# Optimization experiments

Hardware: AMD Instinct MI355X
Metric: run time of the kernel (lower is better)

## Reference

```python
import jax, jax.numpy as jnp
import numpy as np

H_DIM = 1024
HEAD_DIM = 128
N_HEADS = 8
HD = HEAD_DIM * N_HEADS  # 1024


def setup_inputs() -> dict:
    key = jax.random.key(0)
    ks = jax.random.split(key, 32)
    B, S = 16, 1024
    inp = {
        "f_in": jax.random.normal(ks[0], (B, S, H_DIM), jnp.float32),
        "i_in": jax.random.normal(ks[1], (B, S, H_DIM), jnp.float32),
        "z_in": jax.random.normal(ks[2], (B, S, H_DIM), jnp.float32),
        "o_in": jax.random.normal(ks[3], (B, S, H_DIM), jnp.float32),
        "c0": jax.random.normal(ks[4], (B, N_HEADS, HEAD_DIM), jnp.float32),
        "h0": jax.random.normal(ks[5], (B, N_HEADS, HEAD_DIM), jnp.float32),
    }
    # Parameters (torch Linear stored here as [in, out]; init std=0.02, zero bias)
    names_x = ["Fx", "Ix", "Zx", "Ox"]
    names_h = ["Fh", "Ih", "Zh", "Oh"]
    for j, n in enumerate(names_x):
        inp[f"W_{n}"] = 0.02 * jax.random.normal(ks[6 + j], (H_DIM, HD), jnp.float32)
        inp[f"b_{n}"] = jnp.zeros((HD,), jnp.float32)
    for j, n in enumerate(names_h):
        inp[f"W_{n}"] = 0.02 * jax.random.normal(ks[10 + j], (HD, HD), jnp.float32)
        inp[f"b_{n}"] = jnp.zeros((HD,), jnp.float32)
    inp["W_post"] = 0.02 * jax.random.normal(ks[14], (HD, H_DIM), jnp.float32)
    inp["b_post"] = jnp.zeros((H_DIM,), jnp.float32)
    return inp


def reference(f_in, i_in, z_in, o_in, c0, h0,
              W_Fx, b_Fx, W_Ix, b_Ix, W_Zx, b_Zx, W_Ox, b_Ox,
              W_Fh, b_Fh, W_Ih, b_Ih, W_Zh, b_Zh, W_Oh, b_Oh,
              W_post, b_post):
    B, S, _ = f_in.shape
    # Precompute input-to-gate projections for all timesteps: (B,S,HD)
    fx = f_in @ W_Fx + b_Fx
    ix = i_in @ W_Ix + b_Ix
    zx = z_in @ W_Zx + b_Zx
    ox = o_in @ W_Ox + b_Ox
    # Flatten head state: gating is elementwise, heads are contiguous in HD
    c = c0.reshape(B, HD)
    h = h0.reshape(B, HD)
    # Time-major for scan: (S,B,HD)
    xs = (fx.transpose(1, 0, 2), ix.transpose(1, 0, 2),
          zx.transpose(1, 0, 2), ox.transpose(1, 0, 2))

    def step(carry, x):
        c, h = carry
        fx_t, ix_t, zx_t, ox_t = x
        f = jax.nn.sigmoid(fx_t + h @ W_Fh + b_Fh)
        i = jax.nn.sigmoid(ix_t + h @ W_Ih + b_Ih)
        z = jnp.tanh(zx_t + h @ W_Zh + b_Zh)
        o = jax.nn.sigmoid(ox_t + h @ W_Oh + b_Oh)
        c = f * c + i * z
        h = o * jnp.tanh(c)
        return (c, h), h

    (c, h), ys = jax.lax.scan(step, (c, h), xs)
    y = ys.transpose(1, 0, 2)  # (B,S,HD)
    y = y @ W_post + b_post    # n_heads > 1 -> post-head projection
    state = (c.reshape(B, N_HEADS, HEAD_DIM), h.reshape(B, N_HEADS, HEAD_DIM))
    return (y, state)
```

## Files before the change

kernel.cpp:

```cpp
#include <hip/hip_runtime.h>
#include <stdint.h>
#include <stddef.h>

typedef __attribute__((ext_vector_type(8))) short short8;
typedef __attribute__((ext_vector_type(4))) short short4_t;
typedef __attribute__((ext_vector_type(8))) unsigned short ushort8_t;
typedef __attribute__((ext_vector_type(4))) unsigned short ushort4_t;
typedef __attribute__((ext_vector_type(4))) float f32x4;
typedef __attribute__((ext_vector_type(4))) unsigned uint4_t;

#define XG_BYTES  (134217728ull)
#define HS_BYTES  (33587200ull)
#define FLAGS_OFF (XG_BYTES + HS_BYTES)
#define WT_OFF    (FLAGS_OFF + 32768ull)

#define SENT 0x7FC07FC0u

__device__ __forceinline__ unsigned short f2b(float f){
  unsigned u = __builtin_bit_cast(unsigned, f);
  u += 0x7fffu + ((u >> 16) & 1u);
  return (unsigned short)(u >> 16);
}
__device__ __forceinline__ float b2f(unsigned short b){
  unsigned u = ((unsigned)b) << 16;
  return __builtin_bit_cast(float, u);
}
__device__ __forceinline__ float sigm(float x){ return 1.0f / (1.0f + __expf(-x)); }
__device__ __forceinline__ float tanh_(float x){ return 2.0f / (1.0f + __expf(-2.0f*x)) - 1.0f; }

__device__ __forceinline__ void ld_h8_mall(const unsigned short* p, short8* a){
  asm volatile(
    "global_load_dwordx4 %0, %8, off sc0 sc1\n\t"
    "global_load_dwordx4 %1, %8, off offset:64 sc0 sc1\n\t"
    "global_load_dwordx4 %2, %8, off offset:128 sc0 sc1\n\t"
    "global_load_dwordx4 %3, %8, off offset:192 sc0 sc1\n\t"
    "global_load_dwordx4 %4, %8, off offset:256 sc0 sc1\n\t"
    "global_load_dwordx4 %5, %8, off offset:320 sc0 sc1\n\t"
    "global_load_dwordx4 %6, %8, off offset:384 sc0 sc1\n\t"
    "global_load_dwordx4 %7, %8, off offset:448 sc0 sc1\n\t"
    "s_waitcnt vmcnt(0)"
    : "=&v"(a[0]), "=&v"(a[1]), "=&v"(a[2]), "=&v"(a[3]),
      "=&v"(a[4]), "=&v"(a[5]), "=&v"(a[6]), "=&v"(a[7])
    : "v"(p) : "memory");
}
__device__ __forceinline__ void st_u32_mall(unsigned* p, unsigned v){
  asm volatile("global_store_dword %0, %1, off sc0 sc1"
               :: "v"(p), "v"(v) : "memory");
}

__global__ __launch_bounds__(256) void k_prep(
    const float* __restrict__ w0, const float* __restrict__ w1,
    const float* __restrict__ w2, const float* __restrict__ w3,
    const float* __restrict__ w4, const float* __restrict__ w5,
    const float* __restrict__ w6, const float* __restrict__ w7,
    const float* __restrict__ w8, unsigned short* __restrict__ wt)
{
  const int z = blockIdx.z;
  const float* W = (z==0)?w0:(z==1)?w1:(z==2)?w2:(z==3)?w3:(z==4)?w4:
                   (z==5)?w5:(z==6)?w6:(z==7)?w7:w8;
  unsigned short* out = wt + (size_t)z*1024*1024;
  __shared__ float tile[64][65];
  const int k0 = blockIdx.x*64, n0 = blockIdx.y*64;
  const int tid = threadIdx.x;
  {
    const int kk = tid >> 2, nn0 = (tid & 3) * 16;
    const float* src = W + (size_t)(k0+kk)*1024 + n0 + nn0;
    #pragma unroll
    for (int j=0;j<16;j+=4){
      f32x4 v = *(const f32x4*)(src + j);
      tile[kk][nn0+j+0]=v[0]; tile[kk][nn0+j+1]=v[1];
      tile[kk][nn0+j+2]=v[2]; tile[kk][nn0+j+3]=v[3];
    }
  }
  __syncthreads();
  {
    const int nn = tid >> 2, kk0 = (tid & 3) * 16;
    ushort8_t a, b;
    #pragma unroll
    for (int j=0;j<8;++j){ a[j]=f2b(tile[kk0+j][nn]); b[j]=f2b(tile[kk0+8+j][nn]); }
    unsigned short* dst = out + (size_t)(n0+nn)*1024 + k0 + kk0;
    *(ushort8_t*)dst = a;
    *(ushort8_t*)(dst+8) = b;
  }
}

__global__ void k_init(const float* __restrict__ h0, unsigned short* __restrict__ hs){
  const int i = blockIdx.x*256 + threadIdx.x;
  hs[i] = f2b(h0[i]);
}

__global__ void k_fill(unsigned* __restrict__ hsw){
  const size_t i = (size_t)blockIdx.x*256 + threadIdx.x;
  uint4_t v = (uint4_t){SENT, SENT, SENT, SENT};
  *(uint4_t*)(hsw + 8192 + i*4) = v;
}

__global__ __launch_bounds__(256,2) void k_xproj(
    const float* __restrict__ xF, const float* __restrict__ xI,
    const float* __restrict__ xZ, const float* __restrict__ xO,
    const float* __restrict__ bF, const float* __restrict__ bI,
    const float* __restrict__ bZ, const float* __restrict__ bO,
    const unsigned short* __restrict__ Wt,
    unsigned short* __restrict__ xg)
{
  const int g  = blockIdx.z;
  const int tm = blockIdx.x, tn = blockIdx.y;
  const float* X  = (g==0)?xF:(g==1)?xI:(g==2)?xZ:xO;
  const float* Bp = (g==0)?bF:(g==1)?bI:(g==2)?bZ:bO;
  const unsigned short* Wg = Wt + (size_t)g*1024*1024;

  __shared__ unsigned short Asm[128*32];
  __shared__ unsigned short Bsm[128*32];

  const int tid  = threadIdx.x;
  const int lane = tid & 63, wv = tid >> 6;
  const int l15  = lane & 15, lg = lane >> 4;
  const int wy   = wv >> 1,  wx = wv & 1;

  const int rr = tid >> 1, kq = tid & 1;
  const int ar = tm*128 + rr;
  const int ab = ar & 15, as_ = ar >> 4;
  const float* aptr = X + ((size_t)ab*1024 + as_)*1024 + kq*16;
  const unsigned short* bp_ = Wg + (size_t)(tn*128 + rr)*1024 + kq*16;
  const int s0 = kq*2;
  unsigned short* aw0 = &Asm[rr*32 + (((s0  ) ^ (rr&3))<<3)];
  unsigned short* aw1 = &Asm[rr*32 + (((s0+1) ^ (rr&3))<<3)];
  unsigned short* bw0 = &Bsm[rr*32 + (((s0  ) ^ (rr&3))<<3)];
  unsigned short* bw1 = &Bsm[rr*32 + (((s0+1) ^ (rr&3))<<3)];

  f32x4 acc[4][4];
  #pragma unroll
  for (int m=0;m<4;++m)
    #pragma unroll
    for (int q=0;q<4;++q) acc[m][q] = (f32x4){0.f,0.f,0.f,0.f};

  for (int k0=0; k0<1024; k0+=32){
    const float* ap = aptr + k0;
    f32x4 v0 = *(const f32x4*)(ap + 0);
    f32x4 v1 = *(const f32x4*)(ap + 4);
    f32x4 v2 = *(const f32x4*)(ap + 8);
    f32x4 v3 = *(const f32x4*)(ap + 12);
    ushort8_t pa, pb;
    #pragma unroll
    for (int j=0;j<4;++j){ pa[j]=f2b(v0[j]); pa[4+j]=f2b(v1[j]); pb[j]=f2b(v2[j]); pb[4+j]=f2b(v3[j]); }
    *(ushort8_t*)aw0 = pa;
    *(ushort8_t*)aw1 = pb;
    ushort8_t q0 = *(const ushort8_t*)(bp_ + k0);
    ushort8_t q1 = *(const ushort8_t*)(bp_ + k0 + 8);
    *(ushort8_t*)bw0 = q0;
    *(ushort8_t*)bw1 = q1;
    __syncthreads();

    short8 af[4], bf_[4];
    #pragma unroll
    for (int m=0;m<4;++m){
      int row = wy*64 + m*16 + l15;
      af[m] = *(const short8*)&Asm[row*32 + ((lg ^ (row&3))<<3)];
    }
    #pragma unroll
    for (int q=0;q<4;++q){
      int row = wx*64 + q*16 + l15;
      bf_[q] = *(const short8*)&Bsm[row*32 + ((lg ^ (row&3))<<3)];
    }
    #pragma unroll
    for (int m=0;m<4;++m)
      #pragma unroll
      for (int q=0;q<4;++q)
        acc[m][q] = __builtin_amdgcn_mfma_f32_16x16x32_bf16(af[m], bf_[q], acc[m][q], 0,0,0);
    __syncthreads();
  }

  #pragma unroll
  for (int m=0;m<4;++m){
    const int t = tm*8 + wy*4 + m;
    #pragma unroll
    for (int q=0;q<4;++q){
      const int n = tn*128 + wx*64 + q*16 + l15;
      const float bias = Bp[n];
      f32x4 v = acc[m][q];
      ushort4_t pk;
      #pragma unroll
      for (int r=0;r<4;++r) pk[r] = f2b(v[r] + bias);
      *(ushort4_t*)(xg + (size_t)((t*4+g)*1024 + n)*16 + lg*4) = pk;
    }
  }
}

__global__ __launch_bounds__(256,1) void k_recur(
    const unsigned short* __restrict__ WtR,
    const float* __restrict__ bfh, const float* __restrict__ bih,
    const float* __restrict__ bzh, const float* __restrict__ boh,
    const float* __restrict__ c0,
    const unsigned short* __restrict__ xg,
    unsigned short* __restrict__ hs,
    float* __restrict__ oc, float* __restrict__ oh)
{
  const int wg   = blockIdx.x;
  const int tid  = threadIdx.x;
  const int wv   = tid >> 6, lane = tid & 63;
  const int l15  = lane & 15, lg = lane >> 4;
  const int n    = wg*16 + l15;

  short8 wf[4][8];
  #pragma unroll
  for (int g=0; g<4; ++g){
    const unsigned short* wp = WtR + (size_t)g*1048576 + (size_t)n*1024 + wv*256 + lg*8;
    #pragma unroll
    for (int c=0; c<8; ++c)
      wf[g][c] = *(const short8*)(wp + c*32);
  }

  float cst[4]; float bias[4];
  bias[0]=bfh[n]; bias[1]=bih[n]; bias[2]=bzh[n]; bias[3]=boh[n];
  #pragma unroll
  for (int r=0;r<4;++r) cst[r] = c0[(size_t)(lg*4+r)*1024 + n];

  __shared__ f32x4 part[2][4][4][64];

  unsigned* hsw = (unsigned*)hs;

  for (int t=0; t<1024; ++t){
    short4_t xq[4];
    #pragma unroll
    for (int g=0; g<4; ++g)
      xq[g] = *(const short4_t*)(xg + (size_t)((t*4+g)*1024 + n)*16 + lg*4);

    const unsigned short* hp = hs + (size_t)t*16384 + (size_t)l15*1024 + wv*256 + lg*8;
    short8 a[8];
    ld_h8_mall(hp, a);
    for(;;){
      bool bad = false;
      #pragma unroll
      for (int c=0;c<8;++c){
        uint4_t q = __builtin_bit_cast(uint4_t, a[c]);
        bad |= (q[0]==SENT)|(q[1]==SENT)|(q[2]==SENT)|(q[3]==SENT);
      }
      if (!__any(bad)) break;
      __builtin_amdgcn_s_sleep(1);
      ld_h8_mall(hp, a);
    }

    f32x4 acc[4];
    #pragma unroll
    for (int g=0;g<4;++g) acc[g] = (f32x4){0.f,0.f,0.f,0.f};
    #pragma unroll
    for (int c=0;c<8;++c){
      acc[0] = __builtin_amdgcn_mfma_f32_16x16x32_bf16(a[c], wf[0][c], acc[0], 0,0,0);
      acc[1] = __builtin_amdgcn_mfma_f32_16x16x32_bf16(a[c], wf[1][c], acc[1], 0,0,0);
      acc[2] = __builtin_amdgcn_mfma_f32_16x16x32_bf16(a[c], wf[2][c], acc[2], 0,0,0);
      acc[3] = __builtin_amdgcn_mfma_f32_16x16x32_bf16(a[c], wf[3][c], acc[3], 0,0,0);
    }
    const int pb = t & 1;
    #pragma unroll
    for (int g=0;g<4;++g) part[pb][wv][g][lane] = acc[g];
    __syncthreads();

    f32x4 r_[4];
    #pragma unroll
    for (int g=0;g<4;++g){
      f32x4 s0 = part[pb][0][g][lane];
      f32x4 s1 = part[pb][1][g][lane];
      f32x4 s2 = part[pb][2][g][lane];
      f32x4 s3 = part[pb][3][g][lane];
      r_[g] = (s0 + s1) + (s2 + s3);
    }

    float hv[4];
    {
      const int r = wv;
      float pf = r_[0][r] + b2f((unsigned short)xq[0][r]) + bias[0];
      float pi = r_[1][r] + b2f((unsigned short)xq[1][r]) + bias[1];
      float pz = r_[2][r] + b2f((unsigned short)xq[2][r]) + bias[2];
      float po = r_[3][r] + b2f((unsigned short)xq[3][r]) + bias[3];
      float fg = sigm(pf), ig = sigm(pi), zg = tanh_(pz), og = sigm(po);
      float cn = fg*cst[r] + ig*zg;
      cst[r] = cn;
      hv[r] = og * tanh_(cn);
      unsigned m  = (unsigned)f2b(hv[r]);
      unsigned nb = (unsigned)__shfl_xor(m, 1);
      if ((l15 & 1) == 0){
        unsigned word = m | (nb << 16);
        unsigned* pw = hsw + (size_t)(t+1)*8192 + (size_t)(lg*4+wv)*512 + (n >> 1);
        st_u32_mall(pw, word);
      }
    }
    #pragma unroll
    for (int r=0;r<4;++r){
      if (r == wv) continue;
      float pf = r_[0][r] + b2f((unsigned short)xq[0][r]) + bias[0];
      float pi = r_[1][r] + b2f((unsigned short)xq[1][r]) + bias[1];
      float pz = r_[2][r] + b2f((unsigned short)xq[2][r]) + bias[2];
      float po = r_[3][r] + b2f((unsigned short)xq[3][r]) + bias[3];
      float fg = sigm(pf), ig = sigm(pi), zg = tanh_(pz), og = sigm(po);
      float cn = fg*cst[r] + ig*zg;
      cst[r] = cn;
      hv[r] = og * tanh_(cn);
    }
    if (t == 1023 && wv == 0){
      #pragma unroll
      for (int r=0;r<4;++r){
        oc[(size_t)(lg*4+r)*1024 + n] = cst[r];
        oh[(size_t)(lg*4+r)*1024 + n] = hv[r];
      }
    }
  }
}

__global__ __launch_bounds__(256,2) void k_post(
    const unsigned short* __restrict__ hs,
    const unsigned short* __restrict__ Wt,
    const float* __restrict__ bpost,
    float* __restrict__ y)
{
  const int tm = blockIdx.x, tn = blockIdx.y;
  __shared__ unsigned short Asm[128*32];
  __shared__ unsigned short Bsm[128*32];

  const int tid  = threadIdx.x;
  const int lane = tid & 63, wv = tid >> 6;
  const int l15  = lane & 15, lg = lane >> 4;
  const int wy   = wv >> 1,  wx = wv & 1;

  const int rr = tid >> 1, kq = tid & 1;
  const unsigned short* aptr = hs + 16384 + (size_t)(tm*128 + rr)*1024 + kq*16;
  const unsigned short* bp_  = Wt + (size_t)4*1024*1024 + (size_t)(tn*128 + rr)*1024 + kq*16;
  const int s0 = kq*2;
  unsigned short* aw0 = &Asm[rr*32 + (((s0  ) ^ (rr&3))<<3)];
  unsigned short* aw1 = &Asm[rr*32 + (((s0+1) ^ (rr&3))<<3)];
  unsigned short* bw0 = &Bsm[rr*32 + (((s0  ) ^ (rr&3))<<3)];
  unsigned short* bw1 = &Bsm[rr*32 + (((s0+1) ^ (rr&3))<<3)];

  f32x4 acc[4][4];
  #pragma unroll
  for (int m=0;m<4;++m)
    #pragma unroll
    for (int q=0;q<4;++q) acc[m][q] = (f32x4){0.f,0.f,0.f,0.f};

  for (int k0=0; k0<1024; k0+=32){
    ushort8_t a0 = *(const ushort8_t*)(aptr + k0);
    ushort8_t a1 = *(const ushort8_t*)(aptr + k0 + 8);
    *(ushort8_t*)aw0 = a0;
    *(ushort8_t*)aw1 = a1;
    ushort8_t q0 = *(const ushort8_t*)(bp_ + k0);
    ushort8_t q1 = *(const ushort8_t*)(bp_ + k0 + 8);
    *(ushort8_t*)bw0 = q0;
    *(ushort8_t*)bw1 = q1;
    __syncthreads();

    short8 af[4], bf_[4];
    #pragma unroll
    for (int m=0;m<4;++m){
      int row = wy*64 + m*16 + l15;
      af[m] = *(const short8*)&Asm[row*32 + ((lg ^ (row&3))<<3)];
    }
    #pragma unroll
    for (int q=0;q<4;++q){
      int row = wx*64 + q*16 + l15;
      bf_[q] = *(const short8*)&Bsm[row*32 + ((lg ^ (row&3))<<3)];
    }
    #pragma unroll
    for (int m=0;m<4;++m)
      #pragma unroll
      for (int q=0;q<4;++q)
        acc[m][q] = __builtin_amdgcn_mfma_f32_16x16x32_bf16(af[m], bf_[q], acc[m][q], 0,0,0);
    __syncthreads();
  }

  #pragma unroll
  for (int m=0;m<4;++m){
    const int s = tm*8 + wy*4 + m;
    #pragma unroll
    for (int q=0;q<4;++q){
      const int n = tn*128 + wx*64 + q*16 + l15;
      const float bias = bpost[n];
      f32x4 v = acc[m][q];
      #pragma unroll
      for (int r=0;r<4;++r){
        const int b = lg*4 + r;
        y[((size_t)b << 20) + ((size_t)s << 10) + n] = v[r] + bias;
      }
    }
  }
}

extern "C" void kernel_launch(void* const* d_in, const int* in_sizes, int n_in,
                              void* d_out, int out_size, void* d_ws, size_t ws_size,
                              hipStream_t stream)
{
  const float* f_in = (const float*)d_in[0];
  const float* i_in = (const float*)d_in[1];
  const float* z_in = (const float*)d_in[2];
  const float* o_in = (const float*)d_in[3];
  const float* c0   = (const float*)d_in[4];
  const float* h0   = (const float*)d_in[5];
  const float* W_Fx = (const float*)d_in[6];  const float* b_Fx = (const float*)d_in[7];
  const float* W_Ix = (const float*)d_in[8];  const float* b_Ix = (const float*)d_in[9];
  const float* W_Zx = (const float*)d_in[10]; const float* b_Zx = (const float*)d_in[11];
  const float* W_Ox = (const float*)d_in[12]; const float* b_Ox = (const float*)d_in[13];
  const float* W_Fh = (const float*)d_in[14]; const float* b_Fh = (const float*)d_in[15];
  const float* W_Ih = (const float*)d_in[16]; const float* b_Ih = (const float*)d_in[17];
  const float* W_Zh = (const float*)d_in[18]; const float* b_Zh = (const float*)d_in[19];
  const float* W_Oh = (const float*)d_in[20]; const float* b_Oh = (const float*)d_in[21];
  const float* W_post = (const float*)d_in[22]; const float* b_post = (const float*)d_in[23];

  char* ws = (char*)d_ws;
  unsigned short* xg    = (unsigned short*)(ws);
  unsigned short* hs    = (unsigned short*)(ws + XG_BYTES);
  unsigned short* wt    = (unsigned short*)(ws + WT_OFF);

  float* y  = (float*)d_out;
  float* oc = y + 16777216;
  float* oh = oc + 16384;

  k_prep<<<dim3(16,16,9), 256, 0, stream>>>(W_Fx, W_Ix, W_Zx, W_Ox, W_post,
                                            W_Fh, W_Ih, W_Zh, W_Oh, wt);
  k_init<<<64, 256, 0, stream>>>(h0, hs);
  k_fill<<<8192, 256, 0, stream>>>((unsigned*)hs);
  k_xproj<<<dim3(128,8,4), 256, 0, stream>>>(f_in, i_in, z_in, o_in,
                                             b_Fx, b_Ix, b_Zx, b_Ox, wt, xg);
  k_recur<<<64, 256, 0, stream>>>(wt + (size_t)5*1024*1024,
                                  b_Fh, b_Ih, b_Zh, b_Oh,
                                  c0, xg, hs, oc, oh);
  k_post<<<dim3(128,8), 256, 0, stream>>>(hs, wt, b_post, y);
}
```

Baseline: 3.610 ms.

## Halve recurrent workgroups, add per-wave progress flags, prefetch next-step gate inputs

The recurrent kernel now runs on 32 workgroups instead of 64, and each workgroup handles 32 hidden columns, so every wave keeps twice as many weight fragments in registers. This halves the number of producers that must sync each timestep. Each wave gets a specific gate row to finish instead of computing all rows redundantly. Waiters now poll a small progress-flag array rather than sleeping and re-reading the whole h vector. The next timestep's x-projection values are prefetched during the MFMA phase, and the LDS partial-sum layout is changed to scalar floats. In exchange, each workgroup does twice the MFMA work per step and register pressure rises.

```diff
diff --git a/kernel.cpp b/kernel.cpp
--- a/kernel.cpp
+++ b/kernel.cpp
@@ -28,6 +28,13 @@
 __device__ __forceinline__ float sigm(float x){ return 1.0f / (1.0f + __expf(-x)); }
 __device__ __forceinline__ float tanh_(float x){ return 2.0f / (1.0f + __expf(-2.0f*x)) - 1.0f; }
 
+__device__ __forceinline__ unsigned ld_u32_mall(const unsigned* p){
+  unsigned v;
+  asm volatile("global_load_dword %0, %1, off sc0 sc1\n\t"
+               "s_waitcnt vmcnt(0)"
+               : "=v"(v) : "v"(p) : "memory");
+  return v;
+}
 __device__ __forceinline__ void ld_h8_mall(const unsigned short* p, short8* a){
   asm volatile(
     "global_load_dwordx4 %0, %8, off sc0 sc1\n\t"
@@ -193,38 +200,49 @@
     const float* __restrict__ c0,
     const unsigned short* __restrict__ xg,
     unsigned short* __restrict__ hs,
+    unsigned* __restrict__ flags,
     float* __restrict__ oc, float* __restrict__ oh)
 {
   const int wg   = blockIdx.x;
   const int tid  = threadIdx.x;
   const int wv   = tid >> 6, lane = tid & 63;
   const int l15  = lane & 15, lg = lane >> 4;
-  const int n    = wg*16 + l15;
-
-  short8 wf[4][8];
+  const int n0   = wg*32;
+  const int nA   = n0 + l15;
+  const int nB   = n0 + 16 + l15;
+  const int row  = lg*4 + wv;
+  const int sh   = wv * 16;
+
+  short8 wf[4][2][8];
+  #pragma unroll
+  for (int g=0; g<4; ++g)
+    #pragma unroll
+    for (int e=0; e<2; ++e){
+      const unsigned short* wp = WtR + (size_t)g*1048576
+                               + (size_t)(n0 + e*16 + l15)*1024 + wv*256 + lg*8;
+      #pragma unroll
+      for (int c=0; c<8; ++c)
+        wf[g][e][c] = *(const short8*)(wp + c*32);
+    }
+
+  float cstA = c0[(size_t)row*1024 + nA];
+  float cstB = c0[(size_t)row*1024 + nB];
+  float biasA[4] = {bfh[nA], bih[nA], bzh[nA], boh[nA]};
+  float biasB[4] = {bfh[nB], bih[nB], bzh[nB], boh[nB]};
+
+  __shared__ float part[2][4][4][2][4][64];
+
+  unsigned* hsw = (unsigned*)hs;
+
+  short4_t xqA[4], xqB[4];
   #pragma unroll
   for (int g=0; g<4; ++g){
-    const unsigned short* wp = WtR + (size_t)g*1048576 + (size_t)n*1024 + wv*256 + lg*8;
-    #pragma unroll
-    for (int c=0; c<8; ++c)
-      wf[g][c] = *(const short8*)(wp + c*32);
-  }
-
-  float cst[4]; float bias[4];
-  bias[0]=bfh[n]; bias[1]=bih[n]; bias[2]=bzh[n]; bias[3]=boh[n];
-  #pragma unroll
-  for (int r=0;r<4;++r) cst[r] = c0[(size_t)(lg*4+r)*1024 + n];
-
-  __shared__ f32x4 part[2][4][4][64];
-
-  unsigned* hsw = (unsigned*)hs;
-
+    xqA[g] = *(const short4_t*)(xg + (size_t)(g*1024 + nA)*16 + lg*4);
+    xqB[g] = *(const short4_t*)(xg + (size_t)(g*1024 + nB)*16 + lg*4);
+  }
+
+  float hvA = 0.f, hvB = 0.f;
   for (int t=0; t<1024; ++t){
-    short4_t xq[4];
-    #pragma unroll
-    for (int g=0; g<4; ++g)
-      xq[g] = *(const short4_t*)(xg + (size_t)((t*4+g)*1024 + n)*16 + lg*4);
-
     const unsigned short* hp = hs + (size_t)t*16384 + (size_t)l15*1024 + wv*256 + lg*8;
     short8 a[8];
     ld_h8_mall(hp, a);
@@ -236,74 +254,96 @@
         bad |= (q[0]==SENT)|(q[1]==SENT)|(q[2]==SENT)|(q[3]==SENT);
       }
       if (!__any(bad)) break;
-      __builtin_amdgcn_s_sleep(1);
+      unsigned fv;
+      do { fv = ld_u32_mall(flags + wv*32 + (lane & 31)); }
+      while (!__all((int)(fv >= (unsigned)t)));
       ld_h8_mall(hp, a);
     }
 
-    f32x4 acc[4];
-    #pragma unroll
-    for (int g=0;g<4;++g) acc[g] = (f32x4){0.f,0.f,0.f,0.f};
-    #pragma unroll
-    for (int c=0;c<8;++c){
-      acc[0] = __builtin_amdgcn_mfma_f32_16x16x32_bf16(a[c], wf[0][c], acc[0], 0,0,0);
-      acc[1] = __builtin_amdgcn_mfma_f32_16x16x32_bf16(a[c], wf[1][c], acc[1], 0,0,0);
-      acc[2] = __builtin_amdgcn_mfma_f32_16x16x32_bf16(a[c], wf[2][c], acc[2], 0,0,0);
-      acc[3] = __builtin_amdgcn_mfma_f32_16x16x32_bf16(a[c], wf[3][c], acc[3], 0,0,0);
-    }
+    short4_t xqA_n[4], xqB_n[4];
+    if (t < 1023){
+      const size_t tb = (size_t)(t+1)*4096;
+      #pragma unroll
+      for (int g=0; g<4; ++g){
+        xqA_n[g] = *(const short4_t*)(xg + (tb + (size_t)g*1024 + nA)*16 + lg*4);
+        xqB_n[g] = *(const short4_t*)(xg + (tb + (size_t)g*1024 + nB)*16 + lg*4);
+      }
+    }
+
+    f32x4 acc[4][2];
+    #pragma unroll
+    for (int g=0;g<4;++g){ acc[g][0]=(f32x4){0,0,0,0}; acc[g][1]=(f32x4){0,0,0,0}; }
+    #pragma unroll
+    for (int c=0;c<8;++c)
+      #pragma unroll
+      for (int g=0;g<4;++g){
+        acc[g][0] = __builtin_amdgcn_mfma_f32_16x16x32_bf16(a[c], wf[g][0][c], acc[g][0], 0,0,0);
+        acc[g][1] = __builtin_amdgcn_mfma_f32_16x16x32_bf16(a[c], wf[g][1][c], acc[g][1], 0,0,0);
+      }
+
     const int pb = t & 1;
     #pragma unroll
-    for (int g=0;g<4;++g) part[pb][wv][g][lane] = acc[g];
-    __syncthreads();
-
-    f32x4 r_[4];
+    for (int g=0;g<4;++g)
+      #pragma unroll
+      for (int e=0;e<2;++e)
+        #pragma unroll
+        for (int cm=0;cm<4;++cm)
+          part[pb][wv][g][e][cm][lane] = acc[g][e][cm];
+    asm volatile("s_waitcnt lgkmcnt(0)" ::: "memory");
+    __builtin_amdgcn_s_barrier();
+
+    float rgA[4], rgB[4];
     #pragma unroll
     for (int g=0;g<4;++g){
-      f32x4 s0 = part[pb][0][g][lane];
-      f32x4 s1 = part[pb][1][g][lane];
-      f32x4 s2 = part[pb][2][g][lane];
-      f32x4 s3 = part[pb][3][g][lane];
-      r_[g] = (s0 + s1) + (s2 + s3);
-    }
-
-    float hv[4];
+      rgA[g] = part[pb][0][g][0][wv][lane] + part[pb][1][g][0][wv][lane]
+             + part[pb][2][g][0][wv][lane] + part[pb][3][g][0][wv][lane];
+      rgB[g] = part[pb][0][g][1][wv][lane] + part[pb][1][g][1][wv][lane]
+             + part[pb][2][g][1][wv][lane] + part[pb][3][g][1][wv][lane];
+    }
+
     {
-      const int r = wv;
-      float pf = r_[0][r] + b2f((unsigned short)xq[0][r]) + bias[0];
-      float pi = r_[1][r] + b2f((unsigned short)xq[1][r]) + bias[1];
-      float pz = r_[2][r] + b2f((unsigned short)xq[2][r]) + bias[2];
-      float po = r_[3][r] + b2f((unsigned short)xq[3][r]) + bias[3];
+      float pf = rgA[0] + b2f((unsigned short)(__builtin_bit_cast(unsigned long long, xqA[0]) >> sh)) + biasA[0];
+      float pi = rgA[1] + b2f((unsigned short)(__builtin_bit_cast(unsigned long long, xqA[1]) >> sh)) + biasA[1];
+      float pz = rgA[2] + b2f((unsigned short)(__builtin_bit_cast(unsigned long long, xqA[2]) >> sh)) + biasA[2];
+      float po = rgA[3] + b2f((unsigned short)(__builtin_bit_cast(unsigned long long, xqA[3]) >> sh)) + biasA[3];
       float fg = sigm(pf), ig = sigm(pi), zg = tanh_(pz), og = sigm(po);
-      float cn = fg*cst[r] + ig*zg;
-      cst[r] = cn;
-      hv[r] = og * tanh_(cn);
-      unsigned m  = (unsigned)f2b(hv[r]);
-      unsigned nb = (unsigned)__shfl_xor(m, 1);
+      float cn = fg*cstA + ig*zg;
+      cstA = cn;
+      hvA = og * tanh_(cn);
+    }
+    {
+      float pf = rgB[0] + b2f((unsigned short)(__builtin_bit_cast(unsigned long long, xqB[0]) >> sh)) + biasB[0];
+      float pi = rgB[1] + b2f((unsigned short)(__builtin_bit_cast(unsigned long long, xqB[1]) >> sh)) + biasB[1];
+      float pz = rgB[2] + b2f((unsigned short)(__builtin_bit_cast(unsigned long long, xqB[2]) >> sh)) + biasB[2];
+      float po = rgB[3] + b2f((unsigned short)(__builtin_bit_cast(unsigned long long, xqB[3]) >> sh)) + biasB[3];
+      float fg = sigm(pf), ig = sigm(pi), zg = tanh_(pz), og = sigm(po);
+      float cn = fg*cstB + ig*zg;
+      cstB = cn;
+      hvB = og * tanh_(cn);
+    }
+
+    {
+      unsigned mA  = (unsigned)f2b(hvA);
+      unsigned nbA = (unsigned)__shfl_xor(mA, 1);
+      unsigned mB  = (unsigned)f2b(hvB);
+      unsigned nbB = (unsigned)__shfl_xor(mB, 1);
       if ((l15 & 1) == 0){
-        unsigned word = m | (nb << 16);
-        unsigned* pw = hsw + (size_t)(t+1)*8192 + (size_t)(lg*4+wv)*512 + (n >> 1);
-        st_u32_mall(pw, word);
+        unsigned* base = hsw + (size_t)(t+1)*8192 + (size_t)row*512;
+        st_u32_mall(base + (nA >> 1), mA | (nbA << 16));
+        st_u32_mall(base + (nB >> 1), mB | (nbB << 16));
       }
-    }
-    #pragma unroll
-    for (int r=0;r<4;++r){
-      if (r == wv) continue;
-      float pf = r_[0][r] + b2f((unsigned short)xq[0][r]) + bias[0];
-      float pi = r_[1][r] + b2f((unsigned short)xq[1][r]) + bias[1];
-      float pz = r_[2][r] + b2f((unsigned short)xq[2][r]) + bias[2];
-      float po = r_[3][r] + b2f((unsigned short)xq[3][r]) + bias[3];
-      float fg = sigm(pf), ig = sigm(pi), zg = tanh_(pz), og = sigm(po);
-      float cn = fg*cst[r] + ig*zg;
-      cst[r] = cn;
-      hv[r] = og * tanh_(cn);
-    }
-    if (t == 1023 && wv == 0){
-      #pragma unroll
-      for (int r=0;r<4;++r){
-        oc[(size_t)(lg*4+r)*1024 + n] = cst[r];
-        oh[(size_t)(lg*4+r)*1024 + n] = hv[r];
-      }
-    }
-  }
+      if (lane == 0)
+        st_u32_mall(flags + wg*4 + wv, (unsigned)(t+1));
+    }
+
+    #pragma unroll
+    for (int g=0; g<4; ++g){ xqA[g] = xqA_n[g]; xqB[g] = xqB_n[g]; }
+  }
+
+  oc[(size_t)row*1024 + nA] = cstA;
+  oc[(size_t)row*1024 + nB] = cstB;
+  oh[(size_t)row*1024 + nA] = hvA;
+  oh[(size_t)row*1024 + nB] = hvB;
 }
 
 __global__ __launch_bounds__(256,2) void k_post(
@@ -406,20 +446,22 @@
   char* ws = (char*)d_ws;
   unsigned short* xg    = (unsigned short*)(ws);
   unsigned short* hs    = (unsigned short*)(ws + XG_BYTES);
+  unsigned*       flags = (unsigned*)(ws + FLAGS_OFF);
   unsigned short* wt    = (unsigned short*)(ws + WT_OFF);
 
   float* y  = (float*)d_out;
   float* oc = y + 16777216;
   float* oh = oc + 16384;
 
+  hipMemsetAsync(flags, 0, 4096, stream);
   k_prep<<<dim3(16,16,9), 256, 0, stream>>>(W_Fx, W_Ix, W_Zx, W_Ox, W_post,
                                             W_Fh, W_Ih, W_Zh, W_Oh, wt);
   k_init<<<64, 256, 0, stream>>>(h0, hs);
   k_fill<<<8192, 256, 0, stream>>>((unsigned*)hs);
   k_xproj<<<dim3(128,8,4), 256, 0, stream>>>(f_in, i_in, z_in, o_in,
                                              b_Fx, b_Ix, b_Zx, b_Ox, wt, xg);
-  k_recur<<<64, 256, 0, stream>>>(wt + (size_t)5*1024*1024,
+  k_recur<<<32, 256, 0, stream>>>(wt + (size_t)5*1024*1024,
                                   b_Fh, b_Ih, b_Zh, b_Oh,
-                                  c0, xg, hs, oc, oh);
+                                  c0, xg, hs, flags, oc, oh);
   k_post<<<dim3(128,8), 256, 0, stream>>>(hs, wt, b_post, y);
 }
```

Result: slower. 5.070 ms (+40.4%).

## Split gate math per wave, add progress flags, prefetch next-step gate inputs

Applied to the files above, without the earlier changes.

Each wave now computes the gate nonlinearity for only its own batch row instead of redundantly computing all four rows, and the partial-sum exchange goes through scalar-strided LDS. A per-wave progress flag array is published after each h store, and consumers that see sentinels poll the small flag word before re-reading the full h vector. The next timestep's x-gate inputs are prefetched one step ahead, and the final state is written by all waves. The flag polling adds a global store per wave per step, plus extra spin logic that could add latency on the serial critical path.

```diff
diff --git a/kernel.cpp b/kernel.cpp
--- a/kernel.cpp
+++ b/kernel.cpp
@@ -28,6 +28,13 @@
 __device__ __forceinline__ float sigm(float x){ return 1.0f / (1.0f + __expf(-x)); }
 __device__ __forceinline__ float tanh_(float x){ return 2.0f / (1.0f + __expf(-2.0f*x)) - 1.0f; }
 
+__device__ __forceinline__ unsigned ld_u32_mall(const unsigned* p){
+  unsigned v;
+  asm volatile("global_load_dword %0, %1, off sc0 sc1\n\t"
+               "s_waitcnt vmcnt(0)"
+               : "=v"(v) : "v"(p) : "memory");
+  return v;
+}
 __device__ __forceinline__ void ld_h8_mall(const unsigned short* p, short8* a){
   asm volatile(
     "global_load_dwordx4 %0, %8, off sc0 sc1\n\t"
@@ -193,6 +200,7 @@
     const float* __restrict__ c0,
     const unsigned short* __restrict__ xg,
     unsigned short* __restrict__ hs,
+    unsigned* __restrict__ flags,
     float* __restrict__ oc, float* __restrict__ oh)
 {
   const int wg   = blockIdx.x;
@@ -200,6 +208,8 @@
   const int wv   = tid >> 6, lane = tid & 63;
   const int l15  = lane & 15, lg = lane >> 4;
   const int n    = wg*16 + l15;
+  const int row  = lg*4 + wv;
+  const int sh   = wv * 16;
 
   short8 wf[4][8];
   #pragma unroll
@@ -210,34 +220,55 @@
       wf[g][c] = *(const short8*)(wp + c*32);
   }
 
-  float cst[4]; float bias[4];
-  bias[0]=bfh[n]; bias[1]=bih[n]; bias[2]=bzh[n]; bias[3]=boh[n];
-  #pragma unroll
-  for (int r=0;r<4;++r) cst[r] = c0[(size_t)(lg*4+r)*1024 + n];
-
-  __shared__ f32x4 part[2][4][4][64];
+  float cst = c0[(size_t)row*1024 + n];
+  float bias0 = bfh[n], bias1 = bih[n], bias2 = bzh[n], bias3 = boh[n];
+
+  __shared__ float part[2][4][4][4][64];
 
   unsigned* hsw = (unsigned*)hs;
-
+  const unsigned* myflag = flags + wv*64 + lane;
+
+  short4_t xq[4];
+  #pragma unroll
+  for (int g=0; g<4; ++g)
+    xq[g] = *(const short4_t*)(xg + (size_t)(g*1024 + n)*16 + lg*4);
+
+  float hv = 0.f;
   for (int t=0; t<1024; ++t){
-    short4_t xq[4];
-    #pragma unroll
-    for (int g=0; g<4; ++g)
-      xq[g] = *(const short4_t*)(xg + (size_t)((t*4+g)*1024 + n)*16 + lg*4);
-
     const unsigned short* hp = hs + (size_t)t*16384 + (size_t)l15*1024 + wv*256 + lg*8;
     short8 a[8];
     ld_h8_mall(hp, a);
-    for(;;){
+    {
       bool bad = false;
       #pragma unroll
       for (int c=0;c<8;++c){
         uint4_t q = __builtin_bit_cast(uint4_t, a[c]);
         bad |= (q[0]==SENT)|(q[1]==SENT)|(q[2]==SENT)|(q[3]==SENT);
       }
-      if (!__any(bad)) break;
-      __builtin_amdgcn_s_sleep(1);
-      ld_h8_mall(hp, a);
+      if (__any(bad)){
+        unsigned fv;
+        do { fv = ld_u32_mall(myflag); } while (!__all((int)(fv >= (unsigned)t)));
+        ld_h8_mall(hp, a);
+        for(;;){
+          bad = false;
+          #pragma unroll
+          for (int c=0;c<8;++c){
+            uint4_t q = __builtin_bit_cast(uint4_t, a[c]);
+            bad |= (q[0]==SENT)|(q[1]==SENT)|(q[2]==SENT)|(q[3]==SENT);
+          }
+          if (!__any(bad)) break;
+          __builtin_amdgcn_s_sleep(1);
+          ld_h8_mall(hp, a);
+        }
+      }
+    }
+
+    short4_t xq_n[4];
+    if (t < 1023){
+      const size_t tb = (size_t)(t+1)*4096;
+      #pragma unroll
+      for (int g=0; g<4; ++g)
+        xq_n[g] = *(const short4_t*)(xg + (tb + (size_t)g*1024 + n)*16 + lg*4);
     }
 
     f32x4 acc[4];
@@ -250,60 +281,50 @@
       acc[2] = __builtin_amdgcn_mfma_f32_16x16x32_bf16(a[c], wf[2][c], acc[2], 0,0,0);
       acc[3] = __builtin_amdgcn_mfma_f32_16x16x32_bf16(a[c], wf[3][c], acc[3], 0,0,0);
     }
+
     const int pb = t & 1;
     #pragma unroll
-    for (int g=0;g<4;++g) part[pb][wv][g][lane] = acc[g];
-    __syncthreads();
-
-    f32x4 r_[4];
-    #pragma unroll
-    for (int g=0;g<4;++g){
-      f32x4 s0 = part[pb][0][g][lane];
-      f32x4 s1 = part[pb][1][g][lane];
-      f32x4 s2 = part[pb][2][g][lane];
-      f32x4 s3 = part[pb][3][g][lane];
-      r_[g] = (s0 + s1) + (s2 + s3);
-    }
-
-    float hv[4];
+    for (int g=0;g<4;++g)
+      #pragma unroll
+      for (int cm=0;cm<4;++cm)
+        part[pb][wv][g][cm][lane] = acc[g][cm];
+    asm volatile("s_waitcnt lgkmcnt(0)" ::: "memory");
+    __builtin_amdgcn_s_barrier();
+
+    float rg[4];
+    #pragma unroll
+    for (int g=0;g<4;++g)
+      rg[g] = (part[pb][0][g][wv][lane] + part[pb][1][g][wv][lane])
+            + (part[pb][2][g][wv][lane] + part[pb][3][g][wv][lane]);
+
     {
-      const int r = wv;
-      float pf = r_[0][r] + b2f((unsigned short)xq[0][r]) + bias[0];
-      float pi = r_[1][r] + b2f((unsigned short)xq[1][r]) + bias[1];
-      float pz = r_[2][r] + b2f((unsigned short)xq[2][r]) + bias[2];
-      float po = r_[3][r] + b2f((unsigned short)xq[3][r]) + bias[3];
+      float pf = rg[0] + b2f((unsigned short)(__builtin_bit_cast(unsigned long long, xq[0]) >> sh)) + bias0;
+      float pi = rg[1] + b2f((unsigned short)(__builtin_bit_cast(unsigned long long, xq[1]) >> sh)) + bias1;
+      float pz = rg[2] + b2f((unsigned short)(__builtin_bit_cast(unsigned long long, xq[2]) >> sh)) + bias2;
+      float po = rg[3] + b2f((unsigned short)(__builtin_bit_cast(unsigned long long, xq[3]) >> sh)) + bias3;
       float fg = sigm(pf), ig = sigm(pi), zg = tanh_(pz), og = sigm(po);
-      float cn = fg*cst[r] + ig*zg;
-      cst[r] = cn;
-      hv[r] = og * tanh_(cn);
-      unsigned m  = (unsigned)f2b(hv[r]);
+      float cn = fg*cst + ig*zg;
+      cst = cn;
+      hv = og * tanh_(cn);
+    }
+
+    {
+      unsigned m  = (unsigned)f2b(hv);
       unsigned nb = (unsigned)__shfl_xor(m, 1);
       if ((l15 & 1) == 0){
-        unsigned word = m | (nb << 16);
-        unsigned* pw = hsw + (size_t)(t+1)*8192 + (size_t)(lg*4+wv)*512 + (n >> 1);
-        st_u32_mall(pw, word);
+        unsigned* pw = hsw + (size_t)(t+1)*8192 + (size_t)row*512 + (n >> 1);
+        st_u32_mall(pw, m | (nb << 16));
       }
-    }
-    #pragma unroll
-    for (int r=0;r<4;++r){
-      if (r == wv) continue;
-      float pf = r_[0][r] + b2f((unsigned short)xq[0][r]) + bias[0];
-      float pi = r_[1][r] + b2f((unsigned short)xq[1][r]) + bias[1];
-      float pz = r_[2][r] + b2f((unsigned short)xq[2][r]) + bias[2];
-      float po = r_[3][r] + b2f((unsigned short)xq[3][r]) + bias[3];
-      float fg = sigm(pf), ig = sigm(pi), zg = tanh_(pz), og = sigm(po);
-      float cn = fg*cst[r] + ig*zg;
-      cst[r] = cn;
-      hv[r] = og * tanh_(cn);
-    }
-    if (t == 1023 && wv == 0){
-      #pragma unroll
-      for (int r=0;r<4;++r){
-        oc[(size_t)(lg*4+r)*1024 + n] = cst[r];
-        oh[(size_t)(lg*4+r)*1024 + n] = hv[r];
-      }
-    }
-  }
+      if (lane == 0)
+        st_u32_mall(flags + wg*4 + wv, (unsigned)(t+1));
+    }
+
+    #pragma unroll
+    for (int g=0; g<4; ++g) xq[g] = xq_n[g];
+  }
+
+  oc[(size_t)row*1024 + n] = cst;
+  oh[(size_t)row*1024 + n] = hv;
 }
 
 __global__ __launch_bounds__(256,2) void k_post(
@@ -406,12 +427,14 @@
   char* ws = (char*)d_ws;
   unsigned short* xg    = (unsigned short*)(ws);
   unsigned short* hs    = (unsigned short*)(ws + XG_BYTES);
+  unsigned*       flags = (unsigned*)(ws + FLAGS_OFF);
   unsigned short* wt    = (unsigned short*)(ws + WT_OFF);
 
   float* y  = (float*)d_out;
   float* oc = y + 16777216;
   float* oh = oc + 16384;
 
+  hipMemsetAsync(flags, 0, 4096, stream);
   k_prep<<<dim3(16,16,9), 256, 0, stream>>>(W_Fx, W_Ix, W_Zx, W_Ox, W_post,
                                             W_Fh, W_Ih, W_Zh, W_Oh, wt);
   k_init<<<64, 256, 0, stream>>>(h0, hs);
@@ -420,6 +443,6 @@
                                              b_Fx, b_Ix, b_Zx, b_Ox, wt, xg);
   k_recur<<<64, 256, 0, stream>>>(wt + (size_t)5*1024*1024,
                                   b_Fh, b_Ih, b_Zh, b_Oh,
-                                  c0, xg, hs, oc, oh);
+                                  c0, xg, hs, flags, oc, oh);
   k_post<<<dim3(128,8), 256, 0, stream>>>(hs, wt, b_post, y);
 }
```

Measured after the change: 4.441 ms. +23.0%, slower.
